# Optimization experiments

Measured on AMD Instinct MI355X. Metric: run time of the kernel, lower is better.

## Reference

```python
import jax, jax.numpy as jnp
import numpy as np

B, N, C, H = 2, 1024, 1024, 16
D = C // H  # head_dim = 64

def _layernorm(x, g, b):
    m = jnp.mean(x, axis=-1, keepdims=True)
    v = jnp.mean((x - m) ** 2, axis=-1, keepdims=True)
    return (x - m) * jax.lax.rsqrt(v + 1e-5) * g + b

def _proj(x, w, b, g, beta):
    # Linear(C -> 2C) + LayerNorm(2C) + ReLU
    return jax.nn.relu(_layernorm(x @ w + b, g, beta))

def setup_inputs():
    key = jax.random.key(0)
    ks = jax.random.split(key, 9)
    mk = lambda k, shape, s=0.02: jax.random.normal(k, shape, dtype=jnp.float32) * s
    inp = {"x": jax.random.normal(ks[0], (B, N, C), dtype=jnp.float32)}
    for i, name in enumerate(["q", "k", "v"]):
        inp[name + "_w"] = mk(ks[1 + i], (C, 2 * C))
        inp[name + "_b"] = jnp.zeros((2 * C,), jnp.float32)
        inp[name + "_g"] = jnp.ones((2 * C,), jnp.float32)
        inp[name + "_beta"] = jnp.zeros((2 * C,), jnp.float32)
    inp["amp_mix"] = jax.random.normal(ks[7], (H,), dtype=jnp.float32)
    inp["phase_mix"] = jax.random.normal(ks[8], (H,), dtype=jnp.float32)
    return inp

def reference(x, q_w, q_b, q_g, q_beta, k_w, k_b, k_g, k_beta, v_w, v_b, v_g, v_beta, amp_mix, phase_mix):
    q = _proj(x, q_w, q_b, q_g, q_beta).reshape(B, N, H, 2 * D)
    k = _proj(x, k_w, k_b, k_g, k_beta).reshape(B, N, H, 2 * D)
    v = _proj(x, v_w, v_b, v_g, v_beta).reshape(B, N, H, 2 * D)
    qr, qi = q[..., :D], q[..., D:]
    kr, ki = k[..., :D], k[..., D:]
    vr, vi = v[..., :D], v[..., D:]
    # complex qk^H style logits: [B, N, M, H]
    amp = (jnp.einsum('bnhd,bmhd->bnmh', qr, kr)
           - jnp.einsum('bnhd,bmhd->bnmh', qi, ki)) * amp_mix
    ph = (jnp.einsum('bnhd,bmhd->bnmh', qr, ki)
          + jnp.einsum('bnhd,bmhd->bnmh', qi, kr)) * phase_mix
    # attn = amp * exp(i*ph); score = Re * sigmoid(Im)
    score = (amp * jnp.cos(ph)) * jax.nn.sigmoid(amp * jnp.sin(ph))
    attn = jax.nn.softmax(score, axis=2)  # softmax over keys (m)
    out_r = jnp.einsum('bnmh,bmhd->bnhd', attn, vr)
    out_i = jnp.einsum('bnmh,bmhd->bnhd', attn, vi)
    return jnp.concatenate([out_r, out_i], axis=-1).reshape(B, N, 2 * C)
```

## Files before the change

### kernel.cpp

```cpp
#include <hip/hip_runtime.h>
#include <math.h>

#define NSEQ   1024
#define KDIM   1024
#define TWOC   2048
#define NB     65536

typedef float  f32x4  __attribute__((ext_vector_type(4)));
typedef short  short8 __attribute__((ext_vector_type(8)));
typedef short  short4v __attribute__((ext_vector_type(4)));
typedef unsigned int u32x4 __attribute__((ext_vector_type(4)));
typedef __bf16 bf16x8 __attribute__((ext_vector_type(8)));

#define PANROW   40
#define PANHALF  10240
#define PANPAIR  20480
#define NPAN_K   32
#define WPAN_Z_BYTES 10485760u

#define QPLANE   131072
#define KROWB    272
#define KPLANEB  278528
#define VPLANE   131072

#define QPAN_OFF   0ul
#define KPAN_OFF   16777216ul
#define VTPAN_OFF  34603008ul
#define QBUF_OFF   51380224ul
#define KBUF_OFF   68157440ul
#define VBUF_OFF   84934656ul

__device__ __forceinline__ unsigned short bf16_rne(float x) {
    unsigned int u = __float_as_uint(x);
    u += 0x7fffu + ((u >> 16) & 1u);
    return (unsigned short)(u >> 16);
}

__device__ __forceinline__ void gload_lds16(const void* g, void* l) {
    __builtin_amdgcn_global_load_lds(
        (const __attribute__((address_space(1))) unsigned int*)g,
        (__attribute__((address_space(3))) unsigned int*)l, 16, 0, 0);
}

__device__ __forceinline__ bf16x8 bneg(bf16x8 v) {
    u32x4 u = __builtin_bit_cast(u32x4, v);
    u ^= 0x80008000u;
    return __builtin_bit_cast(bf16x8, u);
}

__global__ __launch_bounds__(256)
void split_x(const float* __restrict__ X, unsigned short* __restrict__ Xpan)
{
    const int c  = blockIdx.x * 256 + threadIdx.x;
    const int m  = c >> 7;
    const int k0 = (c & 127) << 3;
    f32x4 v0 = *(const f32x4*)(X + (size_t)m * KDIM + k0);
    f32x4 v1 = *(const f32x4*)(X + (size_t)m * KDIM + k0 + 4);
    float xv[8] = {v0[0],v0[1],v0[2],v0[3],v1[0],v1[1],v1[2],v1[3]};
    short8 h8, l8;
#pragma unroll
    for (int j = 0; j < 8; ++j) {
        unsigned short h = bf16_rne(xv[j]);
        float hf = __uint_as_float((unsigned int)h << 16);
        unsigned short lo = bf16_rne(xv[j] - hf);
        h8[j] = (short)h; l8[j] = (short)lo;
    }
    const int mb = m >> 7, ml = m & 127, ks = k0 >> 5, kl = k0 & 31;
    char* base = (char*)Xpan + (size_t)(mb * NPAN_K + ks) * PANPAIR + ml * 80 + kl * 2;
    *(short8*)base = h8;
    *(short8*)(base + PANHALF) = l8;
}

__global__ __launch_bounds__(256)
void split_w(const float* __restrict__ Wq, const float* __restrict__ Wk,
             const float* __restrict__ Wv, unsigned short* __restrict__ Wpan)
{
    const int z = blockIdx.z;
    const float* W = (z == 0) ? Wq : (z == 1) ? Wk : Wv;
    char* pan = (char*)Wpan + (size_t)z * WPAN_Z_BYTES;

    __shared__ __align__(16) float T[64][36];
    const int t  = threadIdx.x;
    const int nt = blockIdx.x;
    const int kt = blockIdx.y;
    const int kk = t >> 3, cc = (t & 7) * 4;
#pragma unroll
    for (int i = 0; i < 2; ++i) {
        int kr = kk + i * 32;
        *(f32x4*)&T[kr][cc] = *(const f32x4*)(W + (size_t)(kt * 64 + kr) * TWOC + nt * 32 + cc);
    }
    __syncthreads();
    const int n_i = t & 31, kc = t >> 5;
    const int k0 = kc * 8;
    short8 h8, l8;
#pragma unroll
    for (int x = 0; x < 8; ++x) {
        float xv = T[k0 + x][n_i];
        unsigned short h = bf16_rne(xv);
        float hf = __uint_as_float((unsigned int)h << 16);
        unsigned short lo = bf16_rne(xv - hf);
        h8[x] = (short)h; l8[x] = (short)lo;
    }
    const int n_g = nt * 32 + n_i;
    const int nbk = n_g >> 7, nl = n_g & 127;
    const int k_g = kt * 64 + k0;
    const int ks = k_g >> 5, kl = k_g & 31;
    char* base = pan + (size_t)(nbk * NPAN_K + ks) * PANPAIR + nl * 80 + kl * 2;
    *(short8*)base = h8;
    *(short8*)(base + PANHALF) = l8;
}

__global__ __launch_bounds__(256)
void mfma_gemm(const unsigned short* __restrict__ Xpan,
               const unsigned short* __restrict__ Wpan,
               const float* __restrict__ Bq, const float* __restrict__ Bk,
               const float* __restrict__ Bv,
               float* __restrict__ Yq, float* __restrict__ Yk, float* __restrict__ Yv)
{
    __shared__ __align__(16) char AB[40960];
    const int t = threadIdx.x, l = t & 63, w = t >> 6;
    const int wm = w >> 1, wn = w & 1;
    const int nb = blockIdx.x, mb = blockIdx.y, z = blockIdx.z;
    const char* Apan = (const char*)Xpan + (size_t)mb * NPAN_K * PANPAIR;
    const char* Bpan = (const char*)Wpan + (size_t)z * WPAN_Z_BYTES
                                        + (size_t)nb * NPAN_K * PANPAIR;
    const float* bias = (z == 0) ? Bq : (z == 1) ? Bk : Bv;
    float* Y = (z == 0) ? Yq : (z == 1) ? Yk : Yv;

    f32x4 acc[4][4];
#pragma unroll
    for (int i = 0; i < 4; ++i)
#pragma unroll
        for (int j = 0; j < 4; ++j) acc[i][j] = (f32x4){0.f, 0.f, 0.f, 0.f};

    {
#pragma unroll
        for (int r = 0; r < 5; ++r) {
            int off = r * 4096 + t * 16;
            gload_lds16(Apan + off, AB + off);
            gload_lds16(Bpan + off, AB + 20480 + off);
        }
    }
    const int lg  = (l >> 4) * 16;
    const int l15 = l & 15;

    for (int ks = 0; ks < 32; ++ks) {
        __syncthreads();
        short8 ahi[4], alo[4];
#pragma unroll
        for (int fi = 0; fi < 4; ++fi) {
            int row = wm * 64 + fi * 16 + l15;
            ahi[fi] = *(const short8*)(AB + row * 80 + lg);
            alo[fi] = *(const short8*)(AB + PANHALF + row * 80 + lg);
        }
#pragma unroll
        for (int fj = 0; fj < 4; ++fj) {
            int rn = wn * 64 + fj * 16 + l15;
            short8 bh = *(const short8*)(AB + 20480 + rn * 80 + lg);
            short8 bl = *(const short8*)(AB + 30720 + rn * 80 + lg);
            bf16x8 bhv = __builtin_bit_cast(bf16x8, bh);
            bf16x8 blv = __builtin_bit_cast(bf16x8, bl);
#pragma unroll
            for (int fi = 0; fi < 4; ++fi) {
                bf16x8 ahv = __builtin_bit_cast(bf16x8, ahi[fi]);
                bf16x8 alv = __builtin_bit_cast(bf16x8, alo[fi]);
                acc[fi][fj] = __builtin_amdgcn_mfma_f32_16x16x32_bf16(ahv, bhv, acc[fi][fj], 0, 0, 0);
                acc[fi][fj] = __builtin_amdgcn_mfma_f32_16x16x32_bf16(ahv, blv, acc[fi][fj], 0, 0, 0);
                acc[fi][fj] = __builtin_amdgcn_mfma_f32_16x16x32_bf16(alv, bhv, acc[fi][fj], 0, 0, 0);
            }
        }
        __syncthreads();
        if (ks < 31) {
            const char* ga = Apan + (size_t)(ks + 1) * PANPAIR;
            const char* gb = Bpan + (size_t)(ks + 1) * PANPAIR;
#pragma unroll
            for (int r = 0; r < 5; ++r) {
                int off = r * 4096 + t * 16;
                gload_lds16(ga + off, AB + off);
                gload_lds16(gb + off, AB + 20480 + off);
            }
        }
    }

#pragma unroll
    for (int fj = 0; fj < 4; ++fj) {
        int ccol = nb * 128 + wn * 64 + fj * 16 + l15;
        float bb = bias[ccol];
        int hh = ccol >> 7, pp = (ccol >> 6) & 1, d0 = ccol & 63;
        float* ybase = Y + (size_t)(hh * 2 + pp) * NB + d0;
#pragma unroll
        for (int fi = 0; fi < 4; ++fi) {
            int mb4 = mb * 128 + wm * 64 + fi * 16 + (l >> 4) * 4;
#pragma unroll
            for (int r = 0; r < 4; ++r) {
                int mg = mb4 + r;
                int bidx = mg >> 10, n = mg & 1023;
                ybase[(size_t)(bidx * 32) * NB + n * 64] = acc[fi][fj][r] + bb;
            }
        }
    }
}

__global__ __launch_bounds__(256)
void ln_relu(float* __restrict__ Yq, float* __restrict__ Yk, float* __restrict__ Yv,
             const float* __restrict__ Gq, const float* __restrict__ BTq,
             const float* __restrict__ Gk, const float* __restrict__ BTk,
             const float* __restrict__ Gv, const float* __restrict__ BTv,
             unsigned short* __restrict__ Qpan, unsigned short* __restrict__ Kpan)
{
    float* Y; const float* G; const float* Bt;
    if (blockIdx.y == 0)      { Y = Yq; G = Gq; Bt = BTq; }
    else if (blockIdx.y == 1) { Y = Yk; G = Gk; Bt = BTk; }
    else                      { Y = Yv; G = Gv; Bt = BTv; }

    const int r    = blockIdx.x;
    const int bidx = r >> 10;
    const int n    = r & 1023;
    const int t    = threadIdx.x;
    const int e0   = t * 8;
    const int chunk = e0 >> 6;
    const int d     = e0 & 63;

    float* p = Y + (size_t)(bidx * 32 + chunk) * NB + n * 64 + d;
    f32x4 v0 = *(f32x4*)p;
    f32x4 v1 = *(f32x4*)(p + 4);
    float xv[8] = {v0[0],v0[1],v0[2],v0[3],v1[0],v1[1],v1[2],v1[3]};

    __shared__ float red[8];
    float s = 0.f;
#pragma unroll
    for (int j = 0; j < 8; ++j) s += xv[j];
#pragma unroll
    for (int off = 32; off > 0; off >>= 1) s += __shfl_down(s, off);
    const int lane = t & 63, wid = t >> 6;
    if (lane == 0) red[wid] = s;
    __syncthreads();
    const float mean = (red[0] + red[1] + red[2] + red[3]) * (1.f / 2048.f);
    __syncthreads();

    float sq = 0.f;
#pragma unroll
    for (int j = 0; j < 8; ++j) { float dx = xv[j] - mean; sq += dx * dx; }
#pragma unroll
    for (int off = 32; off > 0; off >>= 1) sq += __shfl_down(sq, off);
    if (lane == 0) red[wid] = sq;
    __syncthreads();
    const float var  = (red[0] + red[1] + red[2] + red[3]) * (1.f / 2048.f);
    const float rstd = 1.f / sqrtf(var + 1e-5f);

    float yv[8];
#pragma unroll
    for (int j = 0; j < 8; ++j)
        yv[j] = fmaxf((xv[j] - mean) * rstd * G[e0 + j] + Bt[e0 + j], 0.f);

    if (blockIdx.y == 2) {
        f32x4 o0, o1;
#pragma unroll
        for (int j = 0; j < 4; ++j) { o0[j] = yv[j]; o1[j] = yv[j + 4]; }
        *(f32x4*)p       = o0;
        *(f32x4*)(p + 4) = o1;
        return;
    }

    short8 h8, l8;
#pragma unroll
    for (int j = 0; j < 8; ++j) {
        unsigned short hh = bf16_rne(yv[j]);
        float hf = __uint_as_float((unsigned int)hh << 16);
        unsigned short lo = bf16_rne(yv[j] - hf);
        h8[j] = (short)hh; l8[j] = (short)lo;
    }
    const int bh   = bidx * 16 + (e0 >> 7);
    const int dim0 = e0 & 127;
    if (blockIdx.y == 0) {
        unsigned short* dst = Qpan + ((size_t)(bh * 2) * 1024 + n) * 128 + dim0;
        *(short8*)dst = h8;
        *(short8*)(dst + QPLANE) = l8;
    } else {
        unsigned short* dst = Kpan + ((size_t)(bh * 2) * 1024 + n) * 136 + dim0;
        *(short8*)dst = h8;
        *(short8*)(dst + (size_t)1024 * 136) = l8;
    }
}

__global__ __launch_bounds__(256)
void vsplit(const float* __restrict__ vbuf, unsigned short* __restrict__ Vtpan)
{
    __shared__ __align__(16) float T[32][132];
    const int bh = blockIdx.x, nt = blockIdx.y;
    const int n0 = nt * 32;
    const int t = threadIdx.x;
    {
        const int nl = t >> 3, cg = t & 7;
        const int part = cg >> 2, dq = (cg & 3) * 16;
        const float* src = vbuf + (size_t)(bh * 2 + part) * NB + (n0 + nl) * 64 + dq;
#pragma unroll
        for (int i = 0; i < 4; ++i)
            *(f32x4*)&T[nl][cg * 16 + i * 4] = *(const f32x4*)(src + i * 4);
    }
    __syncthreads();
    const int d2 = t & 127, nh = t >> 7;
    unsigned short hv[16], lv[16];
#pragma unroll
    for (int j = 0; j < 16; ++j) {
        float v = T[nh * 16 + j][d2];
        unsigned short hh = bf16_rne(v);
        float hf = __uint_as_float((unsigned int)hh << 16);
        hv[j] = hh; lv[j] = bf16_rne(v - hf);
    }
    unsigned short* dst = Vtpan + ((size_t)(bh * 2) * 128 + d2) * 1024 + n0 + nh * 16;
    *(short8*)dst = *(short8*)&hv[0];
    *(short8*)(dst + 8) = *(short8*)&hv[8];
    unsigned short* dstl = dst + VPLANE;
    *(short8*)dstl = *(short8*)&lv[0];
    *(short8*)(dstl + 8) = *(short8*)&lv[8];
}

__global__ __launch_bounds__(256)
void attn_mfma(const unsigned short* __restrict__ Qpan,
               const unsigned short* __restrict__ Kpan,
               const unsigned short* __restrict__ Vtpan,
               const float* __restrict__ amp_mix, const float* __restrict__ phase_mix,
               float* __restrict__ Out)
{
    __shared__ __align__(16) char Klds[2 * 8704];
    __shared__ __align__(16) char Vlds[2 * 128 * 80];
    __shared__ __align__(16) char Plds[64 * 80];
    __shared__ float sc_s[64];
    __shared__ float l_s[64];

    const int bid = blockIdx.x;
    const int swz = (bid & 7) * 64 + (bid >> 3);
    const int bh = swz >> 4, qt = swz & 15;
    const int h = bh & 15, bidx = bh >> 4;

    const int t = threadIdx.x, l = t & 63, w = t >> 6;
    const int l15 = l & 15, g = l >> 4;

    const float amix = amp_mix[h], pmix = phase_mix[h];

    bf16x8 Qf[2][4];
    {
        const unsigned short* qb = Qpan + ((size_t)(bh * 2) * 1024 + qt * 64 + w * 16 + l15) * 128
                                 + g * 8;
#pragma unroll
        for (int hf = 0; hf < 2; ++hf)
#pragma unroll
            for (int db = 0; db < 4; ++db)
                Qf[hf][db] = __builtin_bit_cast(bf16x8,
                    *(const short8*)(qb + (size_t)hf * QPLANE + db * 32));
    }

    const char* kbase = (const char*)Kpan + (size_t)(bh * 2) * KPLANEB;
    const unsigned short* vbase = Vtpan + (size_t)(bh * 2) * 128 * 1024 + (size_t)t * 1024;

    f32x4 O[8];
#pragma unroll
    for (int i = 0; i < 8; ++i) O[i] = (f32x4){0.f, 0.f, 0.f, 0.f};
    float m_ = -1e30f, l_ = 0.f;

    short8 vreg[4];

    {
#pragma unroll
        for (int i = 0; i < 4; ++i) {
            int c = t + i * 256;
            int hf = c / 544, rem = c - hf * 544;
            gload_lds16(kbase + (size_t)hf * KPLANEB + rem * 16, Klds + c * 16);
        }
        if (w == 0) {
            int c = 1024 + l;
            int hf = c / 544, rem = c - hf * 544;
            gload_lds16(kbase + (size_t)hf * KPLANEB + rem * 16, Klds + c * 16);
        }
#pragma unroll
        for (int s = 0; s < 4; ++s) vreg[s] = *(const short8*)(vbase + s * 8);
#pragma unroll
        for (int s = 0; s < 4; ++s) *(short8*)(Vlds + t * 80 + s * 16) = vreg[s];
    }

    for (int kt = 0; kt < 32; ++kt) {
        __syncthreads();

        f32x4 aA[2], pA[2];
#pragma unroll
        for (int fi = 0; fi < 2; ++fi) {
            aA[fi] = (f32x4){0.f, 0.f, 0.f, 0.f};
            pA[fi] = (f32x4){0.f, 0.f, 0.f, 0.f};
            const char* kr = Klds + (fi * 16 + l15) * 272 + g * 16;
            bf16x8 Fh[4], Fl[4];
#pragma unroll
            for (int db = 0; db < 4; ++db) {
                Fh[db] = __builtin_bit_cast(bf16x8, *(const short8*)(kr + db * 64));
                Fl[db] = __builtin_bit_cast(bf16x8, *(const short8*)(kr + 8704 + db * 64));
            }
            bf16x8 Nh[2] = { bneg(Fh[2]), bneg(Fh[3]) };
            bf16x8 Nl[2] = { bneg(Fl[2]), bneg(Fl[3]) };
#pragma unroll
            for (int db = 0; db < 4; ++db) {
                bf16x8 Ah = (db < 2) ? Fh[db] : Nh[db - 2];
                bf16x8 Al = (db < 2) ? Fl[db] : Nl[db - 2];
                aA[fi] = __builtin_amdgcn_mfma_f32_16x16x32_bf16(Ah, Qf[0][db], aA[fi], 0, 0, 0);
                aA[fi] = __builtin_amdgcn_mfma_f32_16x16x32_bf16(Ah, Qf[1][db], aA[fi], 0, 0, 0);
                aA[fi] = __builtin_amdgcn_mfma_f32_16x16x32_bf16(Al, Qf[0][db], aA[fi], 0, 0, 0);
                bf16x8 Ph = Fh[db ^ 2];
                bf16x8 Pl = Fl[db ^ 2];
                pA[fi] = __builtin_amdgcn_mfma_f32_16x16x32_bf16(Ph, Qf[0][db], pA[fi], 0, 0, 0);
                pA[fi] = __builtin_amdgcn_mfma_f32_16x16x32_bf16(Ph, Qf[1][db], pA[fi], 0, 0, 0);
                pA[fi] = __builtin_amdgcn_mfma_f32_16x16x32_bf16(Pl, Qf[0][db], pA[fi], 0, 0, 0);
            }
        }

        float sv[2][4];
#pragma unroll
        for (int fi = 0; fi < 2; ++fi)
#pragma unroll
            for (int r = 0; r < 4; ++r) {
                float amp = aA[fi][r] * amix;
                float ph  = pA[fi][r] * pmix;
                float sn, cs;
                __sincosf(ph, &sn, &cs);
                float sig = 1.f / (1.f + __expf(-amp * sn));
                sv[fi][r] = amp * cs * sig;
            }

        float rm = sv[0][0];
#pragma unroll
        for (int fi = 0; fi < 2; ++fi)
#pragma unroll
            for (int r = 0; r < 4; ++r) rm = fmaxf(rm, sv[fi][r]);
        rm = fmaxf(rm, __shfl_xor(rm, 16));
        rm = fmaxf(rm, __shfl_xor(rm, 32));
        const float mn  = fmaxf(m_, rm);
        const float scl = __expf(m_ - mn);
        float pv[2][4];
        float rs = 0.f;
#pragma unroll
        for (int fi = 0; fi < 2; ++fi)
#pragma unroll
            for (int r = 0; r < 4; ++r) { pv[fi][r] = __expf(sv[fi][r] - mn); rs += pv[fi][r]; }
        rs += __shfl_xor(rs, 16);
        rs += __shfl_xor(rs, 32);
        l_ = l_ * scl + rs;
        m_ = mn;

#pragma unroll
        for (int fi = 0; fi < 2; ++fi) {
            short4v pk;
#pragma unroll
            for (int r = 0; r < 4; ++r) pk[r] = (short)bf16_rne(pv[fi][r]);
            *(short4v*)(Plds + (w * 16 + l15) * 80 + fi * 32 + g * 8) = pk;
        }
        if (g == 0) sc_s[w * 16 + l15] = scl;

        __syncthreads();

        if (kt < 31) {
            const char* ks = kbase + (size_t)(kt + 1) * 8704;
#pragma unroll
            for (int i = 0; i < 4; ++i) {
                int c = t + i * 256;
                int hf = c / 544, rem = c - hf * 544;
                gload_lds16(ks + (size_t)hf * (KPLANEB - 0) + rem * 16 - (hf ? (size_t)8704 : 0) + (hf ? (size_t)8704 : 0), Klds + c * 16);
            }
            if (w == 0) {
                int c = 1024 + l;
                int hf = c / 544, rem = c - hf * 544;
                gload_lds16(ks + (size_t)hf * KPLANEB + rem * 16, Klds + c * 16);
            }
#pragma unroll
            for (int s = 0; s < 4; ++s) vreg[s] = *(const short8*)(vbase + (kt + 1) * 32 + s * 8);
        }

        f32x4 scv;
#pragma unroll
        for (int r = 0; r < 4; ++r) scv[r] = sc_s[w * 16 + g * 4 + r];
        bf16x8 Pf = __builtin_bit_cast(bf16x8,
            *(const short8*)(Plds + (w * 16 + l15) * 80 + g * 16));
#pragma unroll
        for (int nt = 0; nt < 8; ++nt) {
            bf16x8 Vh = __builtin_bit_cast(bf16x8,
                *(const short8*)(Vlds + (nt * 16 + l15) * 80 + g * 16));
            bf16x8 Vl = __builtin_bit_cast(bf16x8,
                *(const short8*)(Vlds + (128 * 80) + (nt * 16 + l15) * 80 + g * 16));
            O[nt] *= scv;
            O[nt] = __builtin_amdgcn_mfma_f32_16x16x32_bf16(Pf, Vh, O[nt], 0, 0, 0);
            O[nt] = __builtin_amdgcn_mfma_f32_16x16x32_bf16(Pf, Vl, O[nt], 0, 0, 0);
        }

        __syncthreads();

        if (kt < 31) {
#pragma unroll
            for (int s = 0; s < 4; ++s) *(short8*)(Vlds + t * 80 + s * 16) = vreg[s];
        }
    }

    if (g == 0) l_s[w * 16 + l15] = l_;
    __syncthreads();
    f32x4 invv;
#pragma unroll
    for (int r = 0; r < 4; ++r) invv[r] = 1.f / l_s[w * 16 + g * 4 + r];
#pragma unroll
    for (int nt = 0; nt < 8; ++nt) {
#pragma unroll
        for (int r = 0; r < 4; ++r) {
            const int n = qt * 64 + w * 16 + g * 4 + r;
            Out[(size_t)(bidx * NSEQ + n) * TWOC + h * 128 + nt * 16 + l15] = O[nt][r] * invv[r];
        }
    }
}

extern "C" void kernel_launch(void* const* d_in, const int* in_sizes, int n_in,
                              void* d_out, int out_size, void* d_ws, size_t ws_size,
                              hipStream_t stream) {
    (void)in_sizes; (void)n_in; (void)out_size; (void)ws_size;
    const float* x      = (const float*)d_in[0];
    const float* q_w    = (const float*)d_in[1];
    const float* q_b    = (const float*)d_in[2];
    const float* q_g    = (const float*)d_in[3];
    const float* q_beta = (const float*)d_in[4];
    const float* k_w    = (const float*)d_in[5];
    const float* k_b    = (const float*)d_in[6];
    const float* k_g    = (const float*)d_in[7];
    const float* k_beta = (const float*)d_in[8];
    const float* v_w    = (const float*)d_in[9];
    const float* v_b    = (const float*)d_in[10];
    const float* v_g    = (const float*)d_in[11];
    const float* v_beta = (const float*)d_in[12];
    const float* amp_mix   = (const float*)d_in[13];
    const float* phase_mix = (const float*)d_in[14];

    char* ws = (char*)d_ws;
    unsigned short* Qpan  = (unsigned short*)(ws + QPAN_OFF);
    unsigned short* Kpan  = (unsigned short*)(ws + KPAN_OFF);
    unsigned short* Vtpan = (unsigned short*)(ws + VTPAN_OFF);
    unsigned short* Wpan  = (unsigned short*)(ws + QPAN_OFF);
    float* qbuf = (float*)(ws + QBUF_OFF);
    float* kbuf = (float*)(ws + KBUF_OFF);
    float* vbuf = (float*)(ws + VBUF_OFF);
    unsigned short* Xpan = (unsigned short*)d_out;

    split_x<<<1024, 256, 0, stream>>>(x, Xpan);
    split_w<<<dim3(64, 16, 3), 256, 0, stream>>>(q_w, k_w, v_w, Wpan);
    mfma_gemm<<<dim3(16, 16, 3), 256, 0, stream>>>(
        Xpan, Wpan, q_b, k_b, v_b, qbuf, kbuf, vbuf);
    ln_relu<<<dim3(2048, 3), 256, 0, stream>>>(
        qbuf, kbuf, vbuf, q_g, q_beta, k_g, k_beta, v_g, v_beta, Qpan, Kpan);
    vsplit<<<dim3(32, 32), 256, 0, stream>>>(vbuf, Vtpan);
    attn_mfma<<<512, 256, 0, stream>>>(
        Qpan, Kpan, Vtpan, amp_mix, phase_mix, (float*)d_out);
}
```

Baseline: 321.1 us.

## Double-buffer K/V staging, switch PV to single fp16 MFMA, rework split kernels

The attention loop now double-buffers K and V tiles in LDS, loading them with direct global-to-LDS loads issued ahead of compute, which removes one barrier per iteration and the register round-trip for V. V and P move from a split bf16 hi/lo pair to single fp16, halving the PV MFMAs and the V traffic. The split kernels write full padded panel rows, zeroing the pad slot, and vsplit is rewritten with fp16 output, a larger tile and an LDS transpose. It also adds s_setprio hints and fast reciprocals, at the cost of fp16 precision on P and V.

```diff
diff --git a/kernel.cpp b/kernel.cpp
--- a/kernel.cpp
+++ b/kernel.cpp
@@ -11,6 +11,7 @@
 typedef short  short4v __attribute__((ext_vector_type(4)));
 typedef unsigned int u32x4 __attribute__((ext_vector_type(4)));
 typedef __bf16 bf16x8 __attribute__((ext_vector_type(8)));
+typedef _Float16 half8 __attribute__((ext_vector_type(8)));
 
 #define PANROW   40
 #define PANHALF  10240
@@ -19,9 +20,8 @@
 #define WPAN_Z_BYTES 10485760u
 
 #define QPLANE   131072
-#define KROWB    272
 #define KPLANEB  278528
-#define VPLANE   131072
+#define VPLANEB  262144
 
 #define QPAN_OFF   0ul
 #define KPAN_OFF   16777216ul
@@ -51,9 +51,19 @@
 __global__ __launch_bounds__(256)
 void split_x(const float* __restrict__ X, unsigned short* __restrict__ Xpan)
 {
-    const int c  = blockIdx.x * 256 + threadIdx.x;
-    const int m  = c >> 7;
-    const int k0 = (c & 127) << 3;
+    const int c   = blockIdx.x * 256 + threadIdx.x;
+    const int reg = c / 640;
+    const int cc  = c - reg * 640;
+    const int row = cc / 5, slot = cc - row * 5;
+    char* base = (char*)Xpan + (size_t)reg * PANPAIR + row * 80 + slot * 16;
+    if (slot == 4) {
+        short8 z = (short8){0,0,0,0,0,0,0,0};
+        *(short8*)base = z;
+        *(short8*)(base + PANHALF) = z;
+        return;
+    }
+    const int mb = reg >> 5, ks = reg & 31;
+    const int m = mb * 128 + row, k0 = ks * 32 + slot * 8;
     f32x4 v0 = *(const f32x4*)(X + (size_t)m * KDIM + k0);
     f32x4 v1 = *(const f32x4*)(X + (size_t)m * KDIM + k0 + 4);
     float xv[8] = {v0[0],v0[1],v0[2],v0[3],v1[0],v1[1],v1[2],v1[3]};
@@ -65,8 +75,6 @@
         unsigned short lo = bf16_rne(xv[j] - hf);
         h8[j] = (short)h; l8[j] = (short)lo;
     }
-    const int mb = m >> 7, ml = m & 127, ks = k0 >> 5, kl = k0 & 31;
-    char* base = (char*)Xpan + (size_t)(mb * NPAN_K + ks) * PANPAIR + ml * 80 + kl * 2;
     *(short8*)base = h8;
     *(short8*)(base + PANHALF) = l8;
 }
@@ -83,31 +91,42 @@
     const int t  = threadIdx.x;
     const int nt = blockIdx.x;
     const int kt = blockIdx.y;
-    const int kk = t >> 3, cc = (t & 7) * 4;
+    const int kk = t >> 3, cg = (t & 7) * 4;
 #pragma unroll
     for (int i = 0; i < 2; ++i) {
         int kr = kk + i * 32;
-        *(f32x4*)&T[kr][cc] = *(const f32x4*)(W + (size_t)(kt * 64 + kr) * TWOC + nt * 32 + cc);
+        *(f32x4*)&T[kr][cg] = *(const f32x4*)(W + (size_t)(kt * 64 + kr) * TWOC + nt * 32 + cg);
     }
     __syncthreads();
-    const int n_i = t & 31, kc = t >> 5;
-    const int k0 = kc * 8;
-    short8 h8, l8;
-#pragma unroll
-    for (int x = 0; x < 8; ++x) {
-        float xv = T[k0 + x][n_i];
-        unsigned short h = bf16_rne(xv);
-        float hf = __uint_as_float((unsigned int)h << 16);
-        unsigned short lo = bf16_rne(xv - hf);
-        h8[x] = (short)h; l8[x] = (short)lo;
-    }
-    const int n_g = nt * 32 + n_i;
-    const int nbk = n_g >> 7, nl = n_g & 127;
-    const int k_g = kt * 64 + k0;
-    const int ks = k_g >> 5, kl = k_g & 31;
-    char* base = pan + (size_t)(nbk * NPAN_K + ks) * PANPAIR + nl * 80 + kl * 2;
-    *(short8*)base = h8;
-    *(short8*)(base + PANHALF) = l8;
+
+    const int nbk = nt >> 2, nlb = (nt & 3) * 32;
+#pragma unroll
+    for (int i = 0; i < 2; ++i) {
+        int c = t + i * 256;
+        if (c < 320) {
+            int ksi = (c >= 160) ? 1 : 0;
+            int cc  = c - ksi * 160;
+            int row = cc / 5, slot = cc - row * 5;
+            char* base = pan + (size_t)(nbk * NPAN_K + kt * 2 + ksi) * PANPAIR
+                       + (nlb + row) * 80 + slot * 16;
+            short8 h8, l8;
+            if (slot == 4) {
+                h8 = (short8){0,0,0,0,0,0,0,0};
+                l8 = h8;
+            } else {
+#pragma unroll
+                for (int j = 0; j < 8; ++j) {
+                    float xv = T[ksi * 32 + slot * 8 + j][row];
+                    unsigned short h = bf16_rne(xv);
+                    float hf = __uint_as_float((unsigned int)h << 16);
+                    unsigned short lo = bf16_rne(xv - hf);
+                    h8[j] = (short)h; l8[j] = (short)lo;
+                }
+            }
+            *(short8*)base = h8;
+            *(short8*)(base + PANHALF) = l8;
+        }
+    }
 }
 
 __global__ __launch_bounds__(256)
@@ -284,36 +303,65 @@
 }
 
 __global__ __launch_bounds__(256)
-void vsplit(const float* __restrict__ vbuf, unsigned short* __restrict__ Vtpan)
+void vsplit(const float* __restrict__ vbuf, unsigned short* __restrict__ Vt)
 {
-    __shared__ __align__(16) float T[32][132];
+    __shared__ __align__(16) unsigned short Tb[128][72];
     const int bh = blockIdx.x, nt = blockIdx.y;
-    const int n0 = nt * 32;
+    const int n0 = nt * 64;
     const int t = threadIdx.x;
     {
-        const int nl = t >> 3, cg = t & 7;
-        const int part = cg >> 2, dq = (cg & 3) * 16;
-        const float* src = vbuf + (size_t)(bh * 2 + part) * NB + (n0 + nl) * 64 + dq;
-#pragma unroll
-        for (int i = 0; i < 4; ++i)
-            *(f32x4*)&T[nl][cg * 16 + i * 4] = *(const f32x4*)(src + i * 4);
+        const int p = t >> 7, u = t & 127, l4 = u & 3, nl0 = u >> 2;
+        const float* src0 = vbuf + (size_t)(bh * 2 + p) * NB + (size_t)n0 * 64 + l4 * 16;
+#pragma unroll
+        for (int rep = 0; rep < 2; ++rep) {
+            const int row = nl0 + rep * 32;
+            const float* sp = src0 + (size_t)row * 64;
+            f32x4 a = *(const f32x4*)sp,       b = *(const f32x4*)(sp + 4);
+            f32x4 c = *(const f32x4*)(sp + 8), d = *(const f32x4*)(sp + 12);
+            float vv[16] = {a[0],a[1],a[2],a[3],b[0],b[1],b[2],b[3],
+                            c[0],c[1],c[2],c[3],d[0],d[1],d[2],d[3]};
+#pragma unroll
+            for (int j = 0; j < 16; ++j)
+                Tb[p * 64 + l4 * 16 + j][row] =
+                    __builtin_bit_cast(unsigned short, (_Float16)vv[j]);
+        }
     }
     __syncthreads();
-    const int d2 = t & 127, nh = t >> 7;
-    unsigned short hv[16], lv[16];
-#pragma unroll
-    for (int j = 0; j < 16; ++j) {
-        float v = T[nh * 16 + j][d2];
-        unsigned short hh = bf16_rne(v);
-        float hf = __uint_as_float((unsigned int)hh << 16);
-        hv[j] = hh; lv[j] = bf16_rne(v - hf);
-    }
-    unsigned short* dst = Vtpan + ((size_t)(bh * 2) * 128 + d2) * 1024 + n0 + nh * 16;
-    *(short8*)dst = *(short8*)&hv[0];
-    *(short8*)(dst + 8) = *(short8*)&hv[8];
-    unsigned short* dstl = dst + VPLANE;
-    *(short8*)dstl = *(short8*)&lv[0];
-    *(short8*)(dstl + 8) = *(short8*)&lv[8];
+    const int d2 = t >> 1, sseg = t & 1;
+    unsigned short* dst = Vt + ((size_t)bh * 128 + d2) * 1024 + n0 + sseg * 32;
+#pragma unroll
+    for (int i = 0; i < 4; ++i)
+        *(short8*)(dst + i * 8) = *(const short8*)&Tb[d2][sseg * 32 + i * 8];
+}
+
+__device__ __forceinline__ void stage_K(const char* kplane, int kt, char* dst, int t) {
+#pragma unroll
+    for (int i = 0; i < 4; ++i) {
+        int c = t + i * 256;
+        int hf = (c >= 544) ? 1 : 0;
+        int rem = c - hf * 544;
+        gload_lds16(kplane + (size_t)hf * KPLANEB + (size_t)kt * 8704 + rem * 16,
+                    dst + c * 16);
+    }
+    if (t < 64) {
+        int c = 1024 + t;
+        gload_lds16(kplane + KPLANEB + (size_t)kt * 8704 + (c - 544) * 16,
+                    dst + c * 16);
+    }
+}
+
+__device__ __forceinline__ void stage_V(const char* vplane, int kt, char* dst, int t) {
+#pragma unroll
+    for (int i = 0; i < 2; ++i) {
+        int c = t + i * 256;
+        int r = c / 5, s = c - r * 5; if (s == 4) s = 3;
+        gload_lds16(vplane + (size_t)r * 2048 + kt * 64 + s * 16, dst + c * 16);
+    }
+    if (t < 128) {
+        int c = 512 + t;
+        int r = c / 5, s = c - r * 5; if (s == 4) s = 3;
+        gload_lds16(vplane + (size_t)r * 2048 + kt * 64 + s * 16, dst + c * 16);
+    }
 }
 
 __global__ __launch_bounds__(256)
@@ -323,9 +371,9 @@
                const float* __restrict__ amp_mix, const float* __restrict__ phase_mix,
                float* __restrict__ Out)
 {
-    __shared__ __align__(16) char Klds[2 * 8704];
-    __shared__ __align__(16) char Vlds[2 * 128 * 80];
-    __shared__ __align__(16) char Plds[64 * 80];
+    __shared__ __align__(16) char Klds[2][17408];
+    __shared__ __align__(16) char Vlds[2][10240];
+    __shared__ __align__(16) char Plds[5120];
     __shared__ float sc_s[64];
     __shared__ float l_s[64];
 
@@ -341,8 +389,8 @@
 
     bf16x8 Qf[2][4];
     {
-        const unsigned short* qb = Qpan + ((size_t)(bh * 2) * 1024 + qt * 64 + w * 16 + l15) * 128
-                                 + g * 8;
+        const unsigned short* qb = Qpan
+            + ((size_t)(bh * 2) * 1024 + qt * 64 + w * 16 + l15) * 128 + g * 8;
 #pragma unroll
         for (int hf = 0; hf < 2; ++hf)
 #pragma unroll
@@ -352,42 +400,32 @@
     }
 
     const char* kbase = (const char*)Kpan + (size_t)(bh * 2) * KPLANEB;
-    const unsigned short* vbase = Vtpan + (size_t)(bh * 2) * 128 * 1024 + (size_t)t * 1024;
+    const char* vbase = (const char*)Vtpan + (size_t)bh * VPLANEB;
 
     f32x4 O[8];
 #pragma unroll
     for (int i = 0; i < 8; ++i) O[i] = (f32x4){0.f, 0.f, 0.f, 0.f};
     float m_ = -1e30f, l_ = 0.f;
 
-    short8 vreg[4];
-
-    {
-#pragma unroll
-        for (int i = 0; i < 4; ++i) {
-            int c = t + i * 256;
-            int hf = c / 544, rem = c - hf * 544;
-            gload_lds16(kbase + (size_t)hf * KPLANEB + rem * 16, Klds + c * 16);
-        }
-        if (w == 0) {
-            int c = 1024 + l;
-            int hf = c / 544, rem = c - hf * 544;
-            gload_lds16(kbase + (size_t)hf * KPLANEB + rem * 16, Klds + c * 16);
-        }
-#pragma unroll
-        for (int s = 0; s < 4; ++s) vreg[s] = *(const short8*)(vbase + s * 8);
-#pragma unroll
-        for (int s = 0; s < 4; ++s) *(short8*)(Vlds + t * 80 + s * 16) = vreg[s];
-    }
+    stage_K(kbase, 0, Klds[0], t);
+    stage_V(vbase, 0, Vlds[0], t);
 
     for (int kt = 0; kt < 32; ++kt) {
         __syncthreads();
+        const int buf = kt & 1;
+        if (kt < 31) {
+            stage_K(kbase, kt + 1, Klds[buf ^ 1], t);
+            stage_V(vbase, kt + 1, Vlds[buf ^ 1], t);
+        }
+        const char* Kb = Klds[buf];
 
         f32x4 aA[2], pA[2];
+        __builtin_amdgcn_s_setprio(1);
 #pragma unroll
         for (int fi = 0; fi < 2; ++fi) {
             aA[fi] = (f32x4){0.f, 0.f, 0.f, 0.f};
             pA[fi] = (f32x4){0.f, 0.f, 0.f, 0.f};
-            const char* kr = Klds + (fi * 16 + l15) * 272 + g * 16;
+            const char* kr = Kb + (fi * 16 + l15) * 272 + g * 16;
             bf16x8 Fh[4], Fl[4];
 #pragma unroll
             for (int db = 0; db < 4; ++db) {
@@ -410,6 +448,7 @@
                 pA[fi] = __builtin_amdgcn_mfma_f32_16x16x32_bf16(Pl, Qf[0][db], pA[fi], 0, 0, 0);
             }
         }
+        __builtin_amdgcn_s_setprio(0);
 
         float sv[2][4];
 #pragma unroll
@@ -420,7 +459,7 @@
                 float ph  = pA[fi][r] * pmix;
                 float sn, cs;
                 __sincosf(ph, &sn, &cs);
-                float sig = 1.f / (1.f + __expf(-amp * sn));
+                float sig = __builtin_amdgcn_rcpf(1.f + __expf(-amp * sn));
                 sv[fi][r] = amp * cs * sig;
             }
 
@@ -448,59 +487,38 @@
         for (int fi = 0; fi < 2; ++fi) {
             short4v pk;
 #pragma unroll
-            for (int r = 0; r < 4; ++r) pk[r] = (short)bf16_rne(pv[fi][r]);
+            for (int r = 0; r < 4; ++r)
+                pk[r] = (short)__builtin_bit_cast(unsigned short, (_Float16)pv[fi][r]);
             *(short4v*)(Plds + (w * 16 + l15) * 80 + fi * 32 + g * 8) = pk;
         }
         if (g == 0) sc_s[w * 16 + l15] = scl;
 
-        __syncthreads();
-
-        if (kt < 31) {
-            const char* ks = kbase + (size_t)(kt + 1) * 8704;
-#pragma unroll
-            for (int i = 0; i < 4; ++i) {
-                int c = t + i * 256;
-                int hf = c / 544, rem = c - hf * 544;
-                gload_lds16(ks + (size_t)hf * (KPLANEB - 0) + rem * 16 - (hf ? (size_t)8704 : 0) + (hf ? (size_t)8704 : 0), Klds + c * 16);
-            }
-            if (w == 0) {
-                int c = 1024 + l;
-                int hf = c / 544, rem = c - hf * 544;
-                gload_lds16(ks + (size_t)hf * KPLANEB + rem * 16, Klds + c * 16);
-            }
-#pragma unroll
-            for (int s = 0; s < 4; ++s) vreg[s] = *(const short8*)(vbase + (kt + 1) * 32 + s * 8);
-        }
+        asm volatile("s_waitcnt lgkmcnt(0)" ::: "memory");
+        __builtin_amdgcn_s_barrier();
+        __builtin_amdgcn_sched_barrier(0);
 
         f32x4 scv;
 #pragma unroll
         for (int r = 0; r < 4; ++r) scv[r] = sc_s[w * 16 + g * 4 + r];
-        bf16x8 Pf = __builtin_bit_cast(bf16x8,
+        half8 Pf = __builtin_bit_cast(half8,
             *(const short8*)(Plds + (w * 16 + l15) * 80 + g * 16));
+        const char* Vb = Vlds[buf];
+        __builtin_amdgcn_s_setprio(1);
 #pragma unroll
         for (int nt = 0; nt < 8; ++nt) {
-            bf16x8 Vh = __builtin_bit_cast(bf16x8,
-                *(const short8*)(Vlds + (nt * 16 + l15) * 80 + g * 16));
-            bf16x8 Vl = __builtin_bit_cast(bf16x8,
-                *(const short8*)(Vlds + (128 * 80) + (nt * 16 + l15) * 80 + g * 16));
+            half8 Vh = __builtin_bit_cast(half8,
+                *(const short8*)(Vb + (nt * 16 + l15) * 80 + g * 16));
             O[nt] *= scv;
-            O[nt] = __builtin_amdgcn_mfma_f32_16x16x32_bf16(Pf, Vh, O[nt], 0, 0, 0);
-            O[nt] = __builtin_amdgcn_mfma_f32_16x16x32_bf16(Pf, Vl, O[nt], 0, 0, 0);
-        }
-
-        __syncthreads();
-
-        if (kt < 31) {
-#pragma unroll
-            for (int s = 0; s < 4; ++s) *(short8*)(Vlds + t * 80 + s * 16) = vreg[s];
-        }
+            O[nt] = __builtin_amdgcn_mfma_f32_16x16x32_f16(Pf, Vh, O[nt], 0, 0, 0);
+        }
+        __builtin_amdgcn_s_setprio(0);
     }
 
     if (g == 0) l_s[w * 16 + l15] = l_;
     __syncthreads();
     f32x4 invv;
 #pragma unroll
-    for (int r = 0; r < 4; ++r) invv[r] = 1.f / l_s[w * 16 + g * 4 + r];
+    for (int r = 0; r < 4; ++r) invv[r] = __builtin_amdgcn_rcpf(l_s[w * 16 + g * 4 + r]);
 #pragma unroll
     for (int nt = 0; nt < 8; ++nt) {
 #pragma unroll
@@ -541,13 +559,13 @@
     float* vbuf = (float*)(ws + VBUF_OFF);
     unsigned short* Xpan = (unsigned short*)d_out;
 
-    split_x<<<1024, 256, 0, stream>>>(x, Xpan);
+    split_x<<<1280, 256, 0, stream>>>(x, Xpan);
     split_w<<<dim3(64, 16, 3), 256, 0, stream>>>(q_w, k_w, v_w, Wpan);
     mfma_gemm<<<dim3(16, 16, 3), 256, 0, stream>>>(
         Xpan, Wpan, q_b, k_b, v_b, qbuf, kbuf, vbuf);
     ln_relu<<<dim3(2048, 3), 256, 0, stream>>>(
         qbuf, kbuf, vbuf, q_g, q_beta, k_g, k_beta, v_g, v_beta, Qpan, Kpan);
-    vsplit<<<dim3(32, 32), 256, 0, stream>>>(vbuf, Vtpan);
+    vsplit<<<dim3(32, 16), 256, 0, stream>>>(vbuf, Vtpan);
     attn_mfma<<<512, 256, 0, stream>>>(
         Qpan, Kpan, Vtpan, amp_mix, phase_mix, (float*)d_out);
 }
```

Result: faster. 299.8 us (-6.7%).
